# Kernel optimization log

Hardware: AMD Instinct MI355X
Metric: run time of the kernel (lower is better)

Reference implementation:

```python
import jax, jax.numpy as jnp
import numpy as np

B, T, D, H, E = 16, 4096, 256, 512, 8


def setup_inputs() -> dict:
    key = jax.random.key(0)
    ks = jax.random.split(key, 5)
    x = jax.random.normal(ks[0], (B, T, D), dtype=jnp.float32)
    gate_w = jax.random.normal(ks[1], (D, E), dtype=jnp.float32) * 0.02
    gate_b = jnp.zeros((E,), dtype=jnp.float32)
    W1 = jax.random.normal(ks[2], (E, D, H), dtype=jnp.float32) * 0.02
    b1 = jnp.zeros((E, H), dtype=jnp.float32)
    W2 = jax.random.normal(ks[3], (E, H, D), dtype=jnp.float32) * 0.02
    b2 = jnp.zeros((E, D), dtype=jnp.float32)
    return {"x": x, "gate_w": gate_w, "gate_b": gate_b,
            "W1": W1, "b1": b1, "W2": W2, "b2": b2}


def reference(x, gate_w, gate_b, W1, b1, W2, b2):
    Bb, Tt, Dd = x.shape
    Ee = gate_w.shape[1]
    xf = x.reshape(-1, Dd)                       # [N, D]
    N = xf.shape[0]
    logits = xf @ gate_w + gate_b                # [N, E]
    probs = jax.nn.softmax(logits, axis=-1)
    top2_vals, top2_idx = jax.lax.top_k(probs, 2)  # [N, 2]
    # combine weights: w[n, e] = sum_k top2_vals[n,k] * (top2_idx[n,k]==e)
    cw = jnp.zeros((N, Ee), dtype=xf.dtype).at[
        jnp.arange(N)[:, None], top2_idx].add(top2_vals)  # [N, E]

    def step(acc, params):
        w1, bb1, w2, bb2, we = params            # per-expert slices
        h = jax.nn.gelu(xf @ w1 + bb1, approximate=False)  # [N, H]
        y = h @ w2 + bb2                          # [N, D]
        return acc + we[:, None] * y, None

    out, _ = jax.lax.scan(step, jnp.zeros_like(xf),
                          (W1, b1, W2, b2, cw.T))
    return out.reshape(Bb, Tt, Dd)
```

## Files before the change

### kernel.cpp

```cpp
#include <hip/hip_runtime.h>
#include <hip/hip_bf16.h>
#include <math.h>


#define N_TOK 65536
#define D_DIM 256
#define H_DIM 512
#define E_NUM 8
#define TILE_R 32
#define GRID_TILES 4104

typedef __bf16 bf16x8 __attribute__((ext_vector_type(8)));
typedef float f32x4 __attribute__((ext_vector_type(4)));

static __device__ __forceinline__ ushort f2bf(float f) {
    __hip_bfloat16 h = __float2bfloat16(f);
    ushort u;
    __builtin_memcpy(&u, &h, 2);
    return u;
}

static __device__ __forceinline__ float gelu(float v) {
    const float a = fabsf(v) * 0.70710678118654752f;
    const float t = __builtin_amdgcn_rcpf(fmaf(a, 0.47047f, 1.0f));
    const float p = t * fmaf(t, fmaf(t, 0.7478556f, -0.0958798f), 0.3480242f);
    const float er = fmaf(-p, __expf(-a * a), 1.0f);
    const float s = copysignf(er, v);
    return 0.5f * v * (1.0f + s);
}

__global__ __launch_bounds__(256) void pack_w(const float* __restrict__ W1,
                                              const float* __restrict__ W2,
                                              ushort* __restrict__ W1p,
                                              ushort* __restrict__ W2p) {
    const int t = blockIdx.x * 256 + threadIdx.x;
    const int l = t & 63;
    const int lo = l & 15, hi = l >> 4;
    ushort v[8];
    if (blockIdx.y == 0) {
        const int kb = (t >> 6) & 7;
        const int nb = (t >> 9) & 31;
        const int e  = t >> 14;
        const int k0 = kb * 32 + hi * 8;
        const int n  = nb * 16 + lo;
        const float* src = W1 + (size_t)e * D_DIM * H_DIM + n;
        #pragma unroll
        for (int j = 0; j < 8; ++j)
            v[j] = f2bf(src[(size_t)(k0 + j) * H_DIM]);
        *(uint4*)(W1p + (size_t)t * 8) = *(const uint4*)v;
    } else {
        const int kb = (t >> 6) & 15;
        const int nb = (t >> 10) & 15;
        const int e  = t >> 14;
        const int k0 = kb * 32 + hi * 8;
        const int n  = nb * 16 + lo;
        const float* src = W2 + (size_t)e * H_DIM * D_DIM + n;
        #pragma unroll
        for (int j = 0; j < 8; ++j)
            v[j] = f2bf(src[(size_t)(k0 + j) * D_DIM]);
        *(uint4*)(W2p + (size_t)t * 8) = *(const uint4*)v;
    }
}

__global__ __launch_bounds__(256) void gating(const float* __restrict__ x,
                                              const float* __restrict__ gate_w,
                                              const float* __restrict__ gate_b,
                                              ushort* __restrict__ xb,
                                              int* __restrict__ counts,
                                              int* __restrict__ idx_list,
                                              float* __restrict__ wt_list) {
    __shared__ float gws[2048];
    __shared__ int lc[8];
    __shared__ int lbase[8];

    const int tid = threadIdx.x;
    const size_t t0 = (size_t)blockIdx.x * 64;

    for (int i = tid; i < 2048; i += 256) gws[i] = gate_w[i];
    if (tid < 8) lc[tid] = 0;
    __syncthreads();

    const int m = tid >> 2, q = tid & 3;
    const float4* xr = (const float4*)(x + (t0 + m) * D_DIM + q * 64);
    ushort4* xw = (ushort4*)(xb + (t0 + m) * D_DIM + q * 64);

    double lg[8] = {0, 0, 0, 0, 0, 0, 0, 0};
    #pragma unroll
    for (int it = 0; it < 16; ++it) {
        const float4 v = xr[it];
        ushort4 bv;
        bv.x = f2bf(v.x); bv.y = f2bf(v.y); bv.z = f2bf(v.z); bv.w = f2bf(v.w);
        xw[it] = bv;
        const float* g = &gws[(q * 64 + it * 4) * 8];
        const float vv[4] = {v.x, v.y, v.z, v.w};
        #pragma unroll
        for (int j = 0; j < 4; ++j) {
            const double xv = (double)vv[j];
            #pragma unroll
            for (int e2 = 0; e2 < 8; ++e2) lg[e2] += xv * (double)g[j * 8 + e2];
        }
    }
    #pragma unroll
    for (int e2 = 0; e2 < 8; ++e2) {
        lg[e2] += __shfl_xor(lg[e2], 1, 64);
        lg[e2] += __shfl_xor(lg[e2], 2, 64);
    }

    int e0 = 0, e1 = 0, lp0 = 0, lp1 = 0;
    float p0 = 0.f, p1 = 0.f;
    if (q == 0) {
        #pragma unroll
        for (int e2 = 0; e2 < 8; ++e2) lg[e2] += (double)gate_b[e2];
        double b0 = -1e300, b1v = -1e300;
        #pragma unroll
        for (int e2 = 0; e2 < 8; ++e2)
            if (lg[e2] > b0) { b0 = lg[e2]; e0 = e2; }
        e1 = -1;
        #pragma unroll
        for (int e2 = 0; e2 < 8; ++e2)
            if (e2 != e0 && lg[e2] > b1v) { b1v = lg[e2]; e1 = e2; }
        double s = 0;
        #pragma unroll
        for (int e2 = 0; e2 < 8; ++e2) s += exp(lg[e2] - b0);
        p0 = (float)(1.0 / s);
        p1 = (float)(exp(b1v - b0) / s);
        lp0 = atomicAdd(&lc[e0], 1);
        lp1 = atomicAdd(&lc[e1], 1);
    }
    __syncthreads();
    if (tid < 8) lbase[tid] = atomicAdd(&counts[tid], lc[tid]);
    __syncthreads();
    if (q == 0) {
        const int tok = (int)t0 + m;
        const int o0 = e0 * N_TOK + lbase[e0] + lp0;
        idx_list[o0] = tok; wt_list[o0] = p0;
        const int o1 = e1 * N_TOK + lbase[e1] + lp1;
        idx_list[o1] = tok; wt_list[o1] = p1;
    }
}

__global__ __launch_bounds__(512, 4) void moe_expert(const ushort* __restrict__ xb,
                                                     const ushort* __restrict__ W1p,
                                                     const ushort* __restrict__ W2p,
                                                     const float* __restrict__ b1,
                                                     const float* __restrict__ b2,
                                                     const int* __restrict__ counts,
                                                     const int* __restrict__ idx_list,
                                                     const float* __restrict__ wt_list,
                                                     float* __restrict__ out) {
    __shared__ __align__(16) char U[TILE_R * 1024];
    __shared__ int toks[TILE_R];
    __shared__ float wts[TILE_R];

    const int bid = blockIdx.x;
    const int wg = (bid & 7) * (GRID_TILES / 8) + (bid >> 3);

    int e = -1, row0 = 0, cnt = 0, s = 0;
    #pragma unroll
    for (int i = 0; i < 8; ++i) {
        const int c = counts[i];
        const int nt = (c + TILE_R - 1) >> 5;
        if (e < 0 && wg < s + nt) { e = i; row0 = (wg - s) << 5; cnt = c; }
        s += nt;
    }
    if (e < 0) return;
    const int nval = min(TILE_R, cnt - row0);
    const int tid = threadIdx.x;

    char* Xs = U;
    char* Hs = U;

    const int w = tid >> 6;
    const int l = tid & 63;
    const int lo = l & 15, hi = l >> 4;

    if (tid < TILE_R) {
        const bool vld = tid < nval;
        toks[tid] = vld ? idx_list[e * N_TOK + row0 + tid] : 0;
        wts[tid]  = vld ? wt_list[e * N_TOK + row0 + tid] : 0.0f;
    }

    const char* w1b = (const char*)W1p + (size_t)(e * 32 + w * 4) * 8192 + (size_t)l * 16;
    bf16x8 wf[2][4];
    #pragma unroll
    for (int nb = 0; nb < 4; ++nb)
        wf[0][nb] = *(const bf16x8*)(w1b + nb * 8192);

    __syncthreads();

    {
        const int r = tid >> 4, sb = (tid & 15) * 32;
        const char* src = (const char*)(xb + (size_t)toks[r] * D_DIM);
        char* dst = Xs + r * 512;
        const int sw = (r & 7) << 4;
        *(uint4*)(dst + (sb ^ sw)) = *(const uint4*)(src + sb);
        *(uint4*)(dst + ((sb + 16) ^ sw)) = *(const uint4*)(src + sb + 16);
    }
    __syncthreads();

    f32x4 acc1[4][2];
    #pragma unroll
    for (int nb = 0; nb < 4; ++nb)
        #pragma unroll
        for (int tb = 0; tb < 2; ++tb)
            acc1[nb][tb] = (f32x4){0.f, 0.f, 0.f, 0.f};

    #pragma unroll
    for (int ks = 0; ks < 8; ++ks) {
        const int cur = ks & 1, nxt = cur ^ 1;
        if (ks < 7) {
            #pragma unroll
            for (int nb = 0; nb < 4; ++nb)
                wf[nxt][nb] = *(const bf16x8*)(w1b + nb * 8192 + (ks + 1) * 1024);
        }
        #pragma unroll
        for (int tb = 0; tb < 2; ++tb) {
            const int slot = tb * 16 + lo;
            const bf16x8 xf = *(const bf16x8*)(Xs + slot * 512 +
                              ((ks * 64 + hi * 16) ^ ((slot & 7) << 4)));
            __builtin_amdgcn_s_setprio(1);
            #pragma unroll
            for (int nb = 0; nb < 4; ++nb)
                acc1[nb][tb] = __builtin_amdgcn_mfma_f32_16x16x32_bf16(wf[cur][nb], xf, acc1[nb][tb], 0, 0, 0);
            __builtin_amdgcn_s_setprio(0);
        }
    }

    const char* w2b = (const char*)W2p + (size_t)(e * 16 + w * 2) * 16384 + (size_t)l * 16;
    bf16x8 wf2[2][2];
    wf2[0][0] = *(const bf16x8*)(w2b);
    wf2[0][1] = *(const bf16x8*)(w2b + 16384);

    __syncthreads();

    #pragma unroll
    for (int nb = 0; nb < 4; ++nb) {
        const int hc0 = w * 64 + nb * 16 + hi * 4;
        const float4 b1q = *(const float4*)(b1 + e * H_DIM + hc0);
        #pragma unroll
        for (int tb = 0; tb < 2; ++tb) {
            const int slot = tb * 16 + lo;
            ushort4 hv;
            hv.x = f2bf(gelu(acc1[nb][tb][0] + b1q.x));
            hv.y = f2bf(gelu(acc1[nb][tb][1] + b1q.y));
            hv.z = f2bf(gelu(acc1[nb][tb][2] + b1q.z));
            hv.w = f2bf(gelu(acc1[nb][tb][3] + b1q.w));
            *(ushort4*)(Hs + slot * 1024 + ((hc0 * 2) ^ ((slot & 7) << 4))) = hv;
        }
    }
    __syncthreads();

    f32x4 acc2[2][2];
    #pragma unroll
    for (int mi = 0; mi < 2; ++mi)
        #pragma unroll
        for (int ni = 0; ni < 2; ++ni)
            acc2[mi][ni] = (f32x4){0.f, 0.f, 0.f, 0.f};

    #pragma unroll
    for (int ks = 0; ks < 16; ++ks) {
        const int cur = ks & 1, nxt = cur ^ 1;
        if (ks < 15) {
            wf2[nxt][0] = *(const bf16x8*)(w2b + (ks + 1) * 1024);
            wf2[nxt][1] = *(const bf16x8*)(w2b + 16384 + (ks + 1) * 1024);
        }
        #pragma unroll
        for (int mi = 0; mi < 2; ++mi) {
            const int slot = mi * 16 + lo;
            const bf16x8 hf = *(const bf16x8*)(Hs + slot * 1024 +
                              ((ks * 64 + hi * 16) ^ ((slot & 7) << 4)));
            __builtin_amdgcn_s_setprio(1);
            #pragma unroll
            for (int ni = 0; ni < 2; ++ni)
                acc2[mi][ni] = __builtin_amdgcn_mfma_f32_16x16x32_bf16(hf, wf2[cur][ni], acc2[mi][ni], 0, 0, 0);
            __builtin_amdgcn_s_setprio(0);
        }
    }

    #pragma unroll
    for (int ni = 0; ni < 2; ++ni) {
        const int col = w * 32 + ni * 16 + lo;
        const float b2v = b2[e * D_DIM + col];
        #pragma unroll
        for (int mi = 0; mi < 2; ++mi) {
            #pragma unroll
            for (int rg = 0; rg < 4; ++rg) {
                const int r = mi * 16 + hi * 4 + rg;
                if (r < nval) {
                    const float v = (acc2[mi][ni][rg] + b2v) * wts[r];
                    atomicAdd(&out[(size_t)toks[r] * D_DIM + col], v);
                }
            }
        }
    }
}

extern "C" void kernel_launch(void* const* d_in, const int* in_sizes, int n_in,
                              void* d_out, int out_size, void* d_ws, size_t ws_size,
                              hipStream_t stream) {
    const float* x      = (const float*)d_in[0];
    const float* gate_w = (const float*)d_in[1];
    const float* gate_b = (const float*)d_in[2];
    const float* W1     = (const float*)d_in[3];
    const float* b1     = (const float*)d_in[4];
    const float* W2     = (const float*)d_in[5];
    const float* b2     = (const float*)d_in[6];
    float* out = (float*)d_out;

    char* ws = (char*)d_ws;
    ushort* xb      = (ushort*)(ws);
    ushort* W1p     = (ushort*)(ws + 33554432);
    ushort* W2p     = (ushort*)(ws + 35651584);
    int*    idx_lst = (int*)   (ws + 37748736);
    float*  wt_lst  = (float*) (ws + 39845888);
    int*    counts  = (int*)   (ws + 41943040);

    hipMemsetAsync(counts, 0, 32, stream);
    hipMemsetAsync(d_out, 0, (size_t)out_size * sizeof(float), stream);

    pack_w<<<dim3(512, 2), 256, 0, stream>>>(W1, W2, W1p, W2p);
    gating<<<dim3(1024), 256, 0, stream>>>(x, gate_w, gate_b, xb, counts, idx_lst, wt_lst);
    moe_expert<<<dim3(GRID_TILES), 512, 0, stream>>>(xb, W1p, W2p, b1, b2, counts,
                                                     idx_lst, wt_lst, out);
}
```

Measured before the change: 221.1 us.

## Use persistent expert blocks with double-buffered token gather and merge prep kernels

The expert kernel becomes persistent: 512 blocks each walk a contiguous range of tiles, prefetching the next tile's gathered token rows into a second shared buffer while the current tile computes. The W2 prefetch is deepened to a three-slot register ring. Weight packing, gating and output zeroing are merged into a single prep kernel, which removes the output memset and two extra kernel launches. In exchange, occupancy drops from 4 to 2 blocks per SIMD budget and shared memory use goes up, so fewer independent tiles are in flight to hide latency.

```diff
diff --git a/kernel.cpp b/kernel.cpp
--- a/kernel.cpp
+++ b/kernel.cpp
@@ -8,7 +8,7 @@
 #define H_DIM 512
 #define E_NUM 8
 #define TILE_R 32
-#define GRID_TILES 4104
+#define NBLK 512
 
 typedef __bf16 bf16x8 __attribute__((ext_vector_type(8)));
 typedef float f32x4 __attribute__((ext_vector_type(4)));
@@ -29,53 +29,66 @@
     return 0.5f * v * (1.0f + s);
 }
 
-__global__ __launch_bounds__(256) void pack_w(const float* __restrict__ W1,
-                                              const float* __restrict__ W2,
-                                              ushort* __restrict__ W1p,
-                                              ushort* __restrict__ W2p) {
-    const int t = blockIdx.x * 256 + threadIdx.x;
-    const int l = t & 63;
-    const int lo = l & 15, hi = l >> 4;
-    ushort v[8];
-    if (blockIdx.y == 0) {
-        const int kb = (t >> 6) & 7;
-        const int nb = (t >> 9) & 31;
-        const int e  = t >> 14;
-        const int k0 = kb * 32 + hi * 8;
-        const int n  = nb * 16 + lo;
-        const float* src = W1 + (size_t)e * D_DIM * H_DIM + n;
-        #pragma unroll
-        for (int j = 0; j < 8; ++j)
-            v[j] = f2bf(src[(size_t)(k0 + j) * H_DIM]);
-        *(uint4*)(W1p + (size_t)t * 8) = *(const uint4*)v;
-    } else {
-        const int kb = (t >> 6) & 15;
-        const int nb = (t >> 10) & 15;
-        const int e  = t >> 14;
-        const int k0 = kb * 32 + hi * 8;
-        const int n  = nb * 16 + lo;
-        const float* src = W2 + (size_t)e * H_DIM * D_DIM + n;
-        #pragma unroll
-        for (int j = 0; j < 8; ++j)
-            v[j] = f2bf(src[(size_t)(k0 + j) * D_DIM]);
-        *(uint4*)(W2p + (size_t)t * 8) = *(const uint4*)v;
-    }
-}
-
-__global__ __launch_bounds__(256) void gating(const float* __restrict__ x,
-                                              const float* __restrict__ gate_w,
-                                              const float* __restrict__ gate_b,
-                                              ushort* __restrict__ xb,
-                                              int* __restrict__ counts,
-                                              int* __restrict__ idx_list,
-                                              float* __restrict__ wt_list) {
+__global__ __launch_bounds__(256) void prep(const float* __restrict__ x,
+                                            const float* __restrict__ gate_w,
+                                            const float* __restrict__ gate_b,
+                                            const float* __restrict__ W1,
+                                            const float* __restrict__ W2,
+                                            ushort* __restrict__ xb,
+                                            ushort* __restrict__ W1p,
+                                            ushort* __restrict__ W2p,
+                                            int* __restrict__ counts,
+                                            int* __restrict__ idx_list,
+                                            float* __restrict__ wt_list,
+                                            float* __restrict__ out) {
     __shared__ float gws[2048];
     __shared__ int lc[8];
     __shared__ int lbase[8];
 
+    const int bid = blockIdx.x;
     const int tid = threadIdx.x;
-    const size_t t0 = (size_t)blockIdx.x * 64;
-
+
+    if (bid >= 2048) {
+        float4* o4 = (float4*)out;
+        const size_t idx = (size_t)(bid - 2048) * 256 + tid;
+        #pragma unroll
+        for (int k = 0; k < 32; ++k)
+            o4[idx + (size_t)k * 131072] = (float4){0.f, 0.f, 0.f, 0.f};
+        return;
+    }
+    if (bid >= 1024) {
+        const int pid = bid - 1024;
+        const int t = (pid & 511) * 256 + tid;
+        const int l = t & 63;
+        const int lo = l & 15, hi = l >> 4;
+        ushort v[8];
+        if (pid < 512) {
+            const int kb = (t >> 6) & 7;
+            const int nb = (t >> 9) & 31;
+            const int e  = t >> 14;
+            const int k0 = kb * 32 + hi * 8;
+            const int n  = nb * 16 + lo;
+            const float* src = W1 + (size_t)e * D_DIM * H_DIM + n;
+            #pragma unroll
+            for (int j = 0; j < 8; ++j)
+                v[j] = f2bf(src[(size_t)(k0 + j) * H_DIM]);
+            *(uint4*)(W1p + (size_t)t * 8) = *(const uint4*)v;
+        } else {
+            const int kb = (t >> 6) & 15;
+            const int nb = (t >> 10) & 15;
+            const int e  = t >> 14;
+            const int k0 = kb * 32 + hi * 8;
+            const int n  = nb * 16 + lo;
+            const float* src = W2 + (size_t)e * H_DIM * D_DIM + n;
+            #pragma unroll
+            for (int j = 0; j < 8; ++j)
+                v[j] = f2bf(src[(size_t)(k0 + j) * D_DIM]);
+            *(uint4*)(W2p + (size_t)t * 8) = *(const uint4*)v;
+        }
+        return;
+    }
+
+    const size_t t0 = (size_t)bid * 64;
     for (int i = tid; i < 2048; i += 256) gws[i] = gate_w[i];
     if (tid < 8) lc[tid] = 0;
     __syncthreads();
@@ -139,7 +152,7 @@
     }
 }
 
-__global__ __launch_bounds__(512, 4) void moe_expert(const ushort* __restrict__ xb,
+__global__ __launch_bounds__(512, 2) void moe_expert(const ushort* __restrict__ xb,
                                                      const ushort* __restrict__ W1p,
                                                      const ushort* __restrict__ W2p,
                                                      const float* __restrict__ b1,
@@ -148,150 +161,195 @@
                                                      const int* __restrict__ idx_list,
                                                      const float* __restrict__ wt_list,
                                                      float* __restrict__ out) {
-    __shared__ __align__(16) char U[TILE_R * 1024];
-    __shared__ int toks[TILE_R];
-    __shared__ float wts[TILE_R];
-
-    const int bid = blockIdx.x;
-    const int wg = (bid & 7) * (GRID_TILES / 8) + (bid >> 3);
-
-    int e = -1, row0 = 0, cnt = 0, s = 0;
+    __shared__ __align__(16) char Xs[2][TILE_R * 512];
+    __shared__ __align__(16) char Hs[TILE_R * 1024];
+    __shared__ int   toksb[2][TILE_R];
+    __shared__ float wtsb[2][TILE_R];
+
+    const int tid = threadIdx.x;
+    const int w = tid >> 6, l = tid & 63;
+    const int lo = l & 15, hi = l >> 4;
+
+    int cnts[8];
     #pragma unroll
-    for (int i = 0; i < 8; ++i) {
-        const int c = counts[i];
-        const int nt = (c + TILE_R - 1) >> 5;
-        if (e < 0 && wg < s + nt) { e = i; row0 = (wg - s) << 5; cnt = c; }
-        s += nt;
-    }
-    if (e < 0) return;
-    const int nval = min(TILE_R, cnt - row0);
-    const int tid = threadIdx.x;
-
-    char* Xs = U;
-    char* Hs = U;
-
-    const int w = tid >> 6;
-    const int l = tid & 63;
-    const int lo = l & 15, hi = l >> 4;
+    for (int i = 0; i < 8; ++i) cnts[i] = counts[i];
+    int n = 0;
+    #pragma unroll
+    for (int i = 0; i < 8; ++i) n += (cnts[i] + TILE_R - 1) >> 5;
+
+    const int sb = ((blockIdx.x & 7) << 6) + (blockIdx.x >> 3);
+    const int qq = n >> 9, rr2 = n & (NBLK - 1);
+    const int t_begin = sb * qq + min(sb, rr2);
+    const int t_count = qq + (sb < rr2 ? 1 : 0);
+    if (t_count == 0) return;
+
+    auto resolve = [&](int wg, int& e_, int& r0_, int& nv_) {
+        e_ = -1;
+        int s = 0;
+        #pragma unroll
+        for (int i = 0; i < 8; ++i) {
+            const int nt = (cnts[i] + TILE_R - 1) >> 5;
+            if (e_ < 0 && wg < s + nt) {
+                e_ = i; r0_ = (wg - s) << 5; nv_ = min(TILE_R, cnts[i] - r0_);
+            }
+            s += nt;
+        }
+    };
+
+    int e, row0, nval;
+    resolve(t_begin, e, row0, nval);
 
     if (tid < TILE_R) {
-        const bool vld = tid < nval;
-        toks[tid] = vld ? idx_list[e * N_TOK + row0 + tid] : 0;
-        wts[tid]  = vld ? wt_list[e * N_TOK + row0 + tid] : 0.0f;
-    }
-
-    const char* w1b = (const char*)W1p + (size_t)(e * 32 + w * 4) * 8192 + (size_t)l * 16;
-    bf16x8 wf[2][4];
-    #pragma unroll
-    for (int nb = 0; nb < 4; ++nb)
-        wf[0][nb] = *(const bf16x8*)(w1b + nb * 8192);
-
+        const bool v = tid < nval;
+        toksb[0][tid] = v ? idx_list[e * N_TOK + row0 + tid] : 0;
+        wtsb[0][tid]  = v ? wt_list[e * N_TOK + row0 + tid] : 0.f;
+    }
+    {
+        const int r = tid >> 4;
+        const int tk = idx_list[e * N_TOK + row0 + min(r, nval - 1)];
+        const char* src = (const char*)(xb + (size_t)tk * D_DIM) + (tid & 15) * 32;
+        const int bo = (tid & 15) * 32, sw = (r & 7) << 4;
+        const uint4 a0 = *(const uint4*)src;
+        const uint4 a1 = *(const uint4*)(src + 16);
+        *(uint4*)(Xs[0] + r * 512 + (bo ^ sw)) = a0;
+        *(uint4*)(Xs[0] + r * 512 + ((bo + 16) ^ sw)) = a1;
+    }
     __syncthreads();
 
-    {
-        const int r = tid >> 4, sb = (tid & 15) * 32;
-        const char* src = (const char*)(xb + (size_t)toks[r] * D_DIM);
-        char* dst = Xs + r * 512;
-        const int sw = (r & 7) << 4;
-        *(uint4*)(dst + (sb ^ sw)) = *(const uint4*)(src + sb);
-        *(uint4*)(dst + ((sb + 16) ^ sw)) = *(const uint4*)(src + sb + 16);
-    }
-    __syncthreads();
-
-    f32x4 acc1[4][2];
-    #pragma unroll
-    for (int nb = 0; nb < 4; ++nb)
-        #pragma unroll
-        for (int tb = 0; tb < 2; ++tb)
-            acc1[nb][tb] = (f32x4){0.f, 0.f, 0.f, 0.f};
-
-    #pragma unroll
-    for (int ks = 0; ks < 8; ++ks) {
-        const int cur = ks & 1, nxt = cur ^ 1;
-        if (ks < 7) {
-            #pragma unroll
-            for (int nb = 0; nb < 4; ++nb)
-                wf[nxt][nb] = *(const bf16x8*)(w1b + nb * 8192 + (ks + 1) * 1024);
-        }
-        #pragma unroll
-        for (int tb = 0; tb < 2; ++tb) {
-            const int slot = tb * 16 + lo;
-            const bf16x8 xf = *(const bf16x8*)(Xs + slot * 512 +
-                              ((ks * 64 + hi * 16) ^ ((slot & 7) << 4)));
-            __builtin_amdgcn_s_setprio(1);
-            #pragma unroll
-            for (int nb = 0; nb < 4; ++nb)
-                acc1[nb][tb] = __builtin_amdgcn_mfma_f32_16x16x32_bf16(wf[cur][nb], xf, acc1[nb][tb], 0, 0, 0);
-            __builtin_amdgcn_s_setprio(0);
-        }
-    }
-
-    const char* w2b = (const char*)W2p + (size_t)(e * 16 + w * 2) * 16384 + (size_t)l * 16;
-    bf16x8 wf2[2][2];
-    wf2[0][0] = *(const bf16x8*)(w2b);
-    wf2[0][1] = *(const bf16x8*)(w2b + 16384);
-
-    __syncthreads();
-
-    #pragma unroll
-    for (int nb = 0; nb < 4; ++nb) {
-        const int hc0 = w * 64 + nb * 16 + hi * 4;
-        const float4 b1q = *(const float4*)(b1 + e * H_DIM + hc0);
-        #pragma unroll
-        for (int tb = 0; tb < 2; ++tb) {
-            const int slot = tb * 16 + lo;
-            ushort4 hv;
-            hv.x = f2bf(gelu(acc1[nb][tb][0] + b1q.x));
-            hv.y = f2bf(gelu(acc1[nb][tb][1] + b1q.y));
-            hv.z = f2bf(gelu(acc1[nb][tb][2] + b1q.z));
-            hv.w = f2bf(gelu(acc1[nb][tb][3] + b1q.w));
-            *(ushort4*)(Hs + slot * 1024 + ((hc0 * 2) ^ ((slot & 7) << 4))) = hv;
-        }
-    }
-    __syncthreads();
-
-    f32x4 acc2[2][2];
-    #pragma unroll
-    for (int mi = 0; mi < 2; ++mi)
-        #pragma unroll
-        for (int ni = 0; ni < 2; ++ni)
-            acc2[mi][ni] = (f32x4){0.f, 0.f, 0.f, 0.f};
-
-    #pragma unroll
-    for (int ks = 0; ks < 16; ++ks) {
-        const int cur = ks & 1, nxt = cur ^ 1;
-        if (ks < 15) {
-            wf2[nxt][0] = *(const bf16x8*)(w2b + (ks + 1) * 1024);
-            wf2[nxt][1] = *(const bf16x8*)(w2b + 16384 + (ks + 1) * 1024);
-        }
-        #pragma unroll
-        for (int mi = 0; mi < 2; ++mi) {
-            const int slot = mi * 16 + lo;
-            const bf16x8 hf = *(const bf16x8*)(Hs + slot * 1024 +
-                              ((ks * 64 + hi * 16) ^ ((slot & 7) << 4)));
-            __builtin_amdgcn_s_setprio(1);
+    for (int ti = 0; ti < t_count; ++ti) {
+        const int cur = ti & 1;
+        const char* w1b = (const char*)W1p + (size_t)(e * 32 + w * 4) * 8192 + (size_t)l * 16;
+        const char* w2b = (const char*)W2p + (size_t)(e * 16 + w * 2) * 16384 + (size_t)l * 16;
+
+        f32x4 acc1[4][2];
+        #pragma unroll
+        for (int nb = 0; nb < 4; ++nb)
+            #pragma unroll
+            for (int tb = 0; tb < 2; ++tb)
+                acc1[nb][tb] = (f32x4){0.f, 0.f, 0.f, 0.f};
+
+        bf16x8 wf[2][4];
+        #pragma unroll
+        for (int nb = 0; nb < 4; ++nb)
+            wf[0][nb] = *(const bf16x8*)(w1b + nb * 8192);
+
+        #pragma unroll
+        for (int ks = 0; ks < 8; ++ks) {
+            const int cb = ks & 1, nx = cb ^ 1;
+            if (ks < 7) {
+                #pragma unroll
+                for (int nb = 0; nb < 4; ++nb)
+                    wf[nx][nb] = *(const bf16x8*)(w1b + nb * 8192 + (ks + 1) * 1024);
+            }
+            #pragma unroll
+            for (int tb = 0; tb < 2; ++tb) {
+                const int slot = tb * 16 + lo;
+                const bf16x8 xf = *(const bf16x8*)(Xs[cur] + slot * 512 +
+                                  ((ks * 64 + hi * 16) ^ ((slot & 7) << 4)));
+                __builtin_amdgcn_s_setprio(1);
+                #pragma unroll
+                for (int nb = 0; nb < 4; ++nb)
+                    acc1[nb][tb] = __builtin_amdgcn_mfma_f32_16x16x32_bf16(wf[cb][nb], xf, acc1[nb][tb], 0, 0, 0);
+                __builtin_amdgcn_s_setprio(0);
+            }
+        }
+
+        const bool hasN = (ti + 1 < t_count);
+        int e2 = e, row02 = row0, nv2 = nval;
+        uint4 g0 = {0, 0, 0, 0}, g1 = {0, 0, 0, 0};
+        int ntk = 0; float nwt = 0.f;
+        if (hasN) {
+            resolve(t_begin + ti + 1, e2, row02, nv2);
+            const int r = tid >> 4;
+            const int tk2 = idx_list[e2 * N_TOK + row02 + min(r, nv2 - 1)];
+            const char* src = (const char*)(xb + (size_t)tk2 * D_DIM) + (tid & 15) * 32;
+            g0 = *(const uint4*)src;
+            g1 = *(const uint4*)(src + 16);
+            if (tid < TILE_R) {
+                const bool v = tid < nv2;
+                ntk = v ? idx_list[e2 * N_TOK + row02 + tid] : 0;
+                nwt = v ? wt_list[e2 * N_TOK + row02 + tid] : 0.f;
+            }
+        }
+
+        bf16x8 wf2[3][2];
+        wf2[0][0] = *(const bf16x8*)(w2b);
+        wf2[0][1] = *(const bf16x8*)(w2b + 16384);
+        wf2[1][0] = *(const bf16x8*)(w2b + 1024);
+        wf2[1][1] = *(const bf16x8*)(w2b + 16384 + 1024);
+
+        __syncthreads();
+
+        #pragma unroll
+        for (int nb = 0; nb < 4; ++nb) {
+            const int hc0 = w * 64 + nb * 16 + hi * 4;
+            const float4 b1q = *(const float4*)(b1 + e * H_DIM + hc0);
+            #pragma unroll
+            for (int tb = 0; tb < 2; ++tb) {
+                const int slot = tb * 16 + lo;
+                ushort4 hv;
+                hv.x = f2bf(gelu(acc1[nb][tb][0] + b1q.x));
+                hv.y = f2bf(gelu(acc1[nb][tb][1] + b1q.y));
+                hv.z = f2bf(gelu(acc1[nb][tb][2] + b1q.z));
+                hv.w = f2bf(gelu(acc1[nb][tb][3] + b1q.w));
+                *(ushort4*)(Hs + slot * 1024 + ((hc0 * 2) ^ ((slot & 7) << 4))) = hv;
+            }
+        }
+        if (hasN) {
+            const int r = tid >> 4;
+            const int bo = (tid & 15) * 32, sw = (r & 7) << 4;
+            *(uint4*)(Xs[cur ^ 1] + r * 512 + (bo ^ sw)) = g0;
+            *(uint4*)(Xs[cur ^ 1] + r * 512 + ((bo + 16) ^ sw)) = g1;
+            if (tid < TILE_R) { toksb[cur ^ 1][tid] = ntk; wtsb[cur ^ 1][tid] = nwt; }
+        }
+        __syncthreads();
+
+        f32x4 acc2[2][2];
+        #pragma unroll
+        for (int mi = 0; mi < 2; ++mi)
             #pragma unroll
             for (int ni = 0; ni < 2; ++ni)
-                acc2[mi][ni] = __builtin_amdgcn_mfma_f32_16x16x32_bf16(hf, wf2[cur][ni], acc2[mi][ni], 0, 0, 0);
-            __builtin_amdgcn_s_setprio(0);
-        }
-    }
-
-    #pragma unroll
-    for (int ni = 0; ni < 2; ++ni) {
-        const int col = w * 32 + ni * 16 + lo;
-        const float b2v = b2[e * D_DIM + col];
-        #pragma unroll
-        for (int mi = 0; mi < 2; ++mi) {
-            #pragma unroll
-            for (int rg = 0; rg < 4; ++rg) {
-                const int r = mi * 16 + hi * 4 + rg;
-                if (r < nval) {
-                    const float v = (acc2[mi][ni][rg] + b2v) * wts[r];
-                    atomicAdd(&out[(size_t)toks[r] * D_DIM + col], v);
+                acc2[mi][ni] = (f32x4){0.f, 0.f, 0.f, 0.f};
+
+        #pragma unroll
+        for (int ks = 0; ks < 16; ++ks) {
+            const int cb = ks % 3;
+            if (ks < 14) {
+                const int lb = (ks + 2) % 3;
+                wf2[lb][0] = *(const bf16x8*)(w2b + (ks + 2) * 1024);
+                wf2[lb][1] = *(const bf16x8*)(w2b + 16384 + (ks + 2) * 1024);
+            }
+            #pragma unroll
+            for (int mi = 0; mi < 2; ++mi) {
+                const int slot = mi * 16 + lo;
+                const bf16x8 hf = *(const bf16x8*)(Hs + slot * 1024 +
+                                  ((ks * 64 + hi * 16) ^ ((slot & 7) << 4)));
+                __builtin_amdgcn_s_setprio(1);
+                #pragma unroll
+                for (int ni = 0; ni < 2; ++ni)
+                    acc2[mi][ni] = __builtin_amdgcn_mfma_f32_16x16x32_bf16(hf, wf2[cb][ni], acc2[mi][ni], 0, 0, 0);
+                __builtin_amdgcn_s_setprio(0);
+            }
+        }
+
+        #pragma unroll
+        for (int ni = 0; ni < 2; ++ni) {
+            const int col = w * 32 + ni * 16 + lo;
+            const float b2v = b2[e * D_DIM + col];
+            #pragma unroll
+            for (int mi = 0; mi < 2; ++mi) {
+                #pragma unroll
+                for (int rg = 0; rg < 4; ++rg) {
+                    const int r = mi * 16 + hi * 4 + rg;
+                    if (r < nval) {
+                        const float v = (acc2[mi][ni][rg] + b2v) * wtsb[cur][r];
+                        atomicAdd(&out[(size_t)toksb[cur][r] * D_DIM + col], v);
+                    }
                 }
             }
         }
+
+        e = e2; row0 = row02; nval = nv2;
     }
 }
 
@@ -316,10 +374,8 @@
     int*    counts  = (int*)   (ws + 41943040);
 
     hipMemsetAsync(counts, 0, 32, stream);
-    hipMemsetAsync(d_out, 0, (size_t)out_size * sizeof(float), stream);
-
-    pack_w<<<dim3(512, 2), 256, 0, stream>>>(W1, W2, W1p, W2p);
-    gating<<<dim3(1024), 256, 0, stream>>>(x, gate_w, gate_b, xb, counts, idx_lst, wt_lst);
-    moe_expert<<<dim3(GRID_TILES), 512, 0, stream>>>(xb, W1p, W2p, b1, b2, counts,
-                                                     idx_lst, wt_lst, out);
-}
+    prep<<<dim3(2560), 256, 0, stream>>>(x, gate_w, gate_b, W1, W2,
+                                         xb, W1p, W2p, counts, idx_lst, wt_lst, out);
+    moe_expert<<<dim3(NBLK), 512, 0, stream>>>(xb, W1p, W2p, b1, b2, counts,
+                                               idx_lst, wt_lst, out);
+}
```

Measured after the change: 273.4 us. 1.24x slower.

## Group tokens by expert pair and fuse both experts per tile, dropping atomics

Applied to the files above, without the earlier changes.

Tokens are bucketed by their ordered top-2 expert pair so each tile computes both experts' FFNs for the same tokens. The gate weight is folded into the GELU activations and the second GEMM runs over the concatenated hidden of both experts, accumulating the full output in registers. Results are stored directly instead of atomically added, so the output memset goes away. Weight packing is fused into the gating launch and a separate scatter kernel builds the pair-sorted token lists. This costs more shared memory per block (lower occupancy bound) and an extra small kernel.

```diff
diff --git a/kernel.cpp b/kernel.cpp
--- a/kernel.cpp
+++ b/kernel.cpp
@@ -6,9 +6,8 @@
 #define N_TOK 65536
 #define D_DIM 256
 #define H_DIM 512
-#define E_NUM 8
 #define TILE_R 32
-#define GRID_TILES 4104
+#define GRID_TILES 2112
 
 typedef __bf16 bf16x8 __attribute__((ext_vector_type(8)));
 typedef float f32x4 __attribute__((ext_vector_type(4)));
@@ -29,55 +28,58 @@
     return 0.5f * v * (1.0f + s);
 }
 
-__global__ __launch_bounds__(256) void pack_w(const float* __restrict__ W1,
-                                              const float* __restrict__ W2,
-                                              ushort* __restrict__ W1p,
-                                              ushort* __restrict__ W2p) {
-    const int t = blockIdx.x * 256 + threadIdx.x;
-    const int l = t & 63;
-    const int lo = l & 15, hi = l >> 4;
-    ushort v[8];
-    if (blockIdx.y == 0) {
-        const int kb = (t >> 6) & 7;
-        const int nb = (t >> 9) & 31;
-        const int e  = t >> 14;
-        const int k0 = kb * 32 + hi * 8;
-        const int n  = nb * 16 + lo;
-        const float* src = W1 + (size_t)e * D_DIM * H_DIM + n;
-        #pragma unroll
-        for (int j = 0; j < 8; ++j)
-            v[j] = f2bf(src[(size_t)(k0 + j) * H_DIM]);
-        *(uint4*)(W1p + (size_t)t * 8) = *(const uint4*)v;
-    } else {
-        const int kb = (t >> 6) & 15;
-        const int nb = (t >> 10) & 15;
-        const int e  = t >> 14;
-        const int k0 = kb * 32 + hi * 8;
-        const int n  = nb * 16 + lo;
-        const float* src = W2 + (size_t)e * H_DIM * D_DIM + n;
-        #pragma unroll
-        for (int j = 0; j < 8; ++j)
-            v[j] = f2bf(src[(size_t)(k0 + j) * D_DIM]);
-        *(uint4*)(W2p + (size_t)t * 8) = *(const uint4*)v;
-    }
-}
-
-__global__ __launch_bounds__(256) void gating(const float* __restrict__ x,
-                                              const float* __restrict__ gate_w,
-                                              const float* __restrict__ gate_b,
-                                              ushort* __restrict__ xb,
-                                              int* __restrict__ counts,
-                                              int* __restrict__ idx_list,
-                                              float* __restrict__ wt_list) {
+__global__ __launch_bounds__(256) void prep(const float* __restrict__ x,
+                                            const float* __restrict__ gate_w,
+                                            const float* __restrict__ gate_b,
+                                            const float* __restrict__ W1,
+                                            const float* __restrict__ W2,
+                                            ushort* __restrict__ xb,
+                                            ushort* __restrict__ W1p,
+                                            ushort* __restrict__ W2p,
+                                            int* __restrict__ counts,
+                                            int* __restrict__ pid_arr,
+                                            float2* __restrict__ pw_arr) {
     __shared__ float gws[2048];
-    __shared__ int lc[8];
-    __shared__ int lbase[8];
-
+    __shared__ int lc[64];
+
+    const int bid = blockIdx.x;
     const int tid = threadIdx.x;
-    const size_t t0 = (size_t)blockIdx.x * 64;
-
+
+    if (bid >= 1024) {
+        const int pid = bid - 1024;
+        const int t = (pid & 511) * 256 + tid;
+        const int l = t & 63;
+        const int lo = l & 15, hi = l >> 4;
+        ushort v[8];
+        if (pid < 512) {
+            const int kb = (t >> 6) & 7;
+            const int nb = (t >> 9) & 31;
+            const int e  = t >> 14;
+            const int k0 = kb * 32 + hi * 8;
+            const int n  = nb * 16 + lo;
+            const float* src = W1 + (size_t)e * D_DIM * H_DIM + n;
+            #pragma unroll
+            for (int j = 0; j < 8; ++j)
+                v[j] = f2bf(src[(size_t)(k0 + j) * H_DIM]);
+            *(uint4*)(W1p + (size_t)t * 8) = *(const uint4*)v;
+        } else {
+            const int kb = (t >> 6) & 15;
+            const int nb = (t >> 10) & 15;
+            const int e  = t >> 14;
+            const int k0 = kb * 32 + hi * 8;
+            const int n  = nb * 16 + lo;
+            const float* src = W2 + (size_t)e * H_DIM * D_DIM + n;
+            #pragma unroll
+            for (int j = 0; j < 8; ++j)
+                v[j] = f2bf(src[(size_t)(k0 + j) * D_DIM]);
+            *(uint4*)(W2p + (size_t)t * 8) = *(const uint4*)v;
+        }
+        return;
+    }
+
+    const size_t t0 = (size_t)bid * 64;
     for (int i = tid; i < 2048; i += 256) gws[i] = gate_w[i];
-    if (tid < 8) lc[tid] = 0;
+    if (tid < 64) lc[tid] = 0;
     __syncthreads();
 
     const int m = tid >> 2, q = tid & 3;
@@ -106,173 +108,210 @@
         lg[e2] += __shfl_xor(lg[e2], 2, 64);
     }
 
-    int e0 = 0, e1 = 0, lp0 = 0, lp1 = 0;
-    float p0 = 0.f, p1 = 0.f;
     if (q == 0) {
+        int e0 = 0, e1 = -1;
         #pragma unroll
         for (int e2 = 0; e2 < 8; ++e2) lg[e2] += (double)gate_b[e2];
         double b0 = -1e300, b1v = -1e300;
         #pragma unroll
         for (int e2 = 0; e2 < 8; ++e2)
             if (lg[e2] > b0) { b0 = lg[e2]; e0 = e2; }
-        e1 = -1;
         #pragma unroll
         for (int e2 = 0; e2 < 8; ++e2)
             if (e2 != e0 && lg[e2] > b1v) { b1v = lg[e2]; e1 = e2; }
         double s = 0;
         #pragma unroll
         for (int e2 = 0; e2 < 8; ++e2) s += exp(lg[e2] - b0);
-        p0 = (float)(1.0 / s);
-        p1 = (float)(exp(b1v - b0) / s);
-        lp0 = atomicAdd(&lc[e0], 1);
-        lp1 = atomicAdd(&lc[e1], 1);
-    }
-    __syncthreads();
-    if (tid < 8) lbase[tid] = atomicAdd(&counts[tid], lc[tid]);
-    __syncthreads();
-    if (q == 0) {
+        const float p0 = (float)(1.0 / s);
+        const float p1 = (float)(exp(b1v - b0) / s);
+        const int pid = e0 * 8 + e1;
+        atomicAdd(&lc[pid], 1);
         const int tok = (int)t0 + m;
-        const int o0 = e0 * N_TOK + lbase[e0] + lp0;
-        idx_list[o0] = tok; wt_list[o0] = p0;
-        const int o1 = e1 * N_TOK + lbase[e1] + lp1;
-        idx_list[o1] = tok; wt_list[o1] = p1;
-    }
-}
-
-__global__ __launch_bounds__(512, 4) void moe_expert(const ushort* __restrict__ xb,
+        pid_arr[tok] = pid;
+        pw_arr[tok] = make_float2(p0, p1);
+    }
+    __syncthreads();
+    if (tid < 64 && lc[tid]) atomicAdd(&counts[tid], lc[tid]);
+}
+
+__global__ __launch_bounds__(256) void scatter(const int* __restrict__ counts,
+                                               const int* __restrict__ pid_arr,
+                                               const float2* __restrict__ pw_arr,
+                                               int* __restrict__ cursor,
+                                               int* __restrict__ tok_list,
+                                               float* __restrict__ w0l,
+                                               float* __restrict__ w1l) {
+    __shared__ int lcnt[64];
+    __shared__ int lbase[64];
+    const int tid = threadIdx.x;
+    const int t = blockIdx.x * 256 + tid;
+    if (tid < 64) lcnt[tid] = 0;
+    __syncthreads();
+    const int pid = pid_arr[t];
+    const float2 pw = pw_arr[t];
+    const int lpos = atomicAdd(&lcnt[pid], 1);
+    __syncthreads();
+    if (tid < 64) {
+        int s = 0;
+        for (int i = 0; i < tid; ++i) s += counts[i];
+        const int mine = lcnt[tid];
+        lbase[tid] = s + (mine ? atomicAdd(&cursor[tid], mine) : 0);
+    }
+    __syncthreads();
+    const int pos = lbase[pid] + lpos;
+    tok_list[pos] = t;
+    w0l[pos] = pw.x;
+    w1l[pos] = pw.y;
+}
+
+__global__ __launch_bounds__(512, 3) void moe_expert(const ushort* __restrict__ xb,
                                                      const ushort* __restrict__ W1p,
                                                      const ushort* __restrict__ W2p,
                                                      const float* __restrict__ b1,
                                                      const float* __restrict__ b2,
                                                      const int* __restrict__ counts,
-                                                     const int* __restrict__ idx_list,
-                                                     const float* __restrict__ wt_list,
+                                                     const int* __restrict__ tok_list,
+                                                     const float* __restrict__ w0l,
+                                                     const float* __restrict__ w1l,
                                                      float* __restrict__ out) {
-    __shared__ __align__(16) char U[TILE_R * 1024];
-    __shared__ int toks[TILE_R];
-    __shared__ float wts[TILE_R];
-
-    const int bid = blockIdx.x;
-    const int wg = (bid & 7) * (GRID_TILES / 8) + (bid >> 3);
-
-    int e = -1, row0 = 0, cnt = 0, s = 0;
-    #pragma unroll
-    for (int i = 0; i < 8; ++i) {
+    __shared__ __align__(16) char Xs[TILE_R * 512];
+    __shared__ __align__(16) char Hs[TILE_R * 2048];
+
+    int n = 0;
+    for (int i = 0; i < 64; ++i) n += (counts[i] + 31) >> 5;
+    const int qn = n >> 3, rn = n & 7;
+    const int xc = blockIdx.x & 7, ix = blockIdx.x >> 3;
+    if (ix >= qn + (xc < rn ? 1 : 0)) return;
+    const int wg = xc * qn + min(xc, rn) + ix;
+
+    int pid = -1, row0 = 0, nv = 0, gbase = 0;
+    int st = 0, sc = 0;
+    for (int i = 0; i < 64; ++i) {
         const int c = counts[i];
-        const int nt = (c + TILE_R - 1) >> 5;
-        if (e < 0 && wg < s + nt) { e = i; row0 = (wg - s) << 5; cnt = c; }
-        s += nt;
-    }
-    if (e < 0) return;
-    const int nval = min(TILE_R, cnt - row0);
+        const int nt = (c + 31) >> 5;
+        if (pid < 0 && wg < st + nt) { pid = i; row0 = (wg - st) << 5; nv = min(TILE_R, c - row0); gbase = sc; }
+        st += nt; sc += c;
+    }
+    const int ea = pid >> 3, eb = pid & 7;
+    const int gidx = gbase + row0;
+
     const int tid = threadIdx.x;
-
-    char* Xs = U;
-    char* Hs = U;
-
-    const int w = tid >> 6;
-    const int l = tid & 63;
+    const int w = tid >> 6, l = tid & 63;
     const int lo = l & 15, hi = l >> 4;
-
-    if (tid < TILE_R) {
-        const bool vld = tid < nval;
-        toks[tid] = vld ? idx_list[e * N_TOK + row0 + tid] : 0;
-        wts[tid]  = vld ? wt_list[e * N_TOK + row0 + tid] : 0.0f;
-    }
-
-    const char* w1b = (const char*)W1p + (size_t)(e * 32 + w * 4) * 8192 + (size_t)l * 16;
-    bf16x8 wf[2][4];
-    #pragma unroll
-    for (int nb = 0; nb < 4; ++nb)
-        wf[0][nb] = *(const bf16x8*)(w1b + nb * 8192);
-
-    __syncthreads();
+    const int qe = w >> 2, pp = w & 3;
+    const int ew = qe ? eb : ea;
+
+    const float* wl = qe ? w1l : w0l;
+    const float wtv0 = wl[gidx + min(lo, nv - 1)];
+    const float wtv1 = wl[gidx + min(16 + lo, nv - 1)];
 
     {
-        const int r = tid >> 4, sb = (tid & 15) * 32;
-        const char* src = (const char*)(xb + (size_t)toks[r] * D_DIM);
-        char* dst = Xs + r * 512;
-        const int sw = (r & 7) << 4;
-        *(uint4*)(dst + (sb ^ sw)) = *(const uint4*)(src + sb);
-        *(uint4*)(dst + ((sb + 16) ^ sw)) = *(const uint4*)(src + sb + 16);
-    }
-    __syncthreads();
-
-    f32x4 acc1[4][2];
-    #pragma unroll
-    for (int nb = 0; nb < 4; ++nb)
-        #pragma unroll
-        for (int tb = 0; tb < 2; ++tb)
-            acc1[nb][tb] = (f32x4){0.f, 0.f, 0.f, 0.f};
-
-    #pragma unroll
-    for (int ks = 0; ks < 8; ++ks) {
-        const int cur = ks & 1, nxt = cur ^ 1;
-        if (ks < 7) {
-            #pragma unroll
-            for (int nb = 0; nb < 4; ++nb)
-                wf[nxt][nb] = *(const bf16x8*)(w1b + nb * 8192 + (ks + 1) * 1024);
-        }
-        #pragma unroll
-        for (int tb = 0; tb < 2; ++tb) {
-            const int slot = tb * 16 + lo;
-            const bf16x8 xf = *(const bf16x8*)(Xs + slot * 512 +
+        const int r = tid >> 4;
+        const int tk = tok_list[gidx + min(r, nv - 1)];
+        const char* src = (const char*)(xb + (size_t)tk * D_DIM) + (tid & 15) * 32;
+        const int bo = (tid & 15) * 32, sw = (r & 7) << 4;
+        const uint4 a0 = *(const uint4*)src;
+        const uint4 a1 = *(const uint4*)(src + 16);
+        *(uint4*)(Xs + r * 512 + (bo ^ sw)) = a0;
+        *(uint4*)(Xs + r * 512 + ((bo + 16) ^ sw)) = a1;
+    }
+    __syncthreads();
+
+    #pragma unroll
+    for (int hh = 0; hh < 2; ++hh) {
+        const int nbg0 = pp * 8 + hh * 4;
+        const char* w1b = (const char*)W1p + (size_t)(ew * 32 + nbg0) * 8192 + (size_t)l * 16;
+
+        f32x4 acc1[4][2];
+        #pragma unroll
+        for (int nb = 0; nb < 4; ++nb)
+            #pragma unroll
+            for (int tb = 0; tb < 2; ++tb)
+                acc1[nb][tb] = (f32x4){0.f, 0.f, 0.f, 0.f};
+
+        bf16x8 wf[2][4];
+        #pragma unroll
+        for (int nb = 0; nb < 4; ++nb)
+            wf[0][nb] = *(const bf16x8*)(w1b + nb * 8192);
+
+        #pragma unroll
+        for (int ks = 0; ks < 8; ++ks) {
+            const int cb = ks & 1, nx = cb ^ 1;
+            if (ks < 7) {
+                #pragma unroll
+                for (int nb = 0; nb < 4; ++nb)
+                    wf[nx][nb] = *(const bf16x8*)(w1b + nb * 8192 + (ks + 1) * 1024);
+            }
+            #pragma unroll
+            for (int tb = 0; tb < 2; ++tb) {
+                const int slot = tb * 16 + lo;
+                const bf16x8 xf = *(const bf16x8*)(Xs + slot * 512 +
+                                  ((ks * 64 + hi * 16) ^ ((slot & 7) << 4)));
+                __builtin_amdgcn_s_setprio(1);
+                #pragma unroll
+                for (int nb = 0; nb < 4; ++nb)
+                    acc1[nb][tb] = __builtin_amdgcn_mfma_f32_16x16x32_bf16(wf[cb][nb], xf, acc1[nb][tb], 0, 0, 0);
+                __builtin_amdgcn_s_setprio(0);
+            }
+        }
+
+        #pragma unroll
+        for (int nb = 0; nb < 4; ++nb) {
+            const int hc = nbg0 * 16 + nb * 16 + hi * 4;
+            const float4 b1q = *(const float4*)(b1 + ew * H_DIM + hc);
+            const int hgc = qe * H_DIM + hc;
+            #pragma unroll
+            for (int tb = 0; tb < 2; ++tb) {
+                const int slot = tb * 16 + lo;
+                const float wt = tb ? wtv1 : wtv0;
+                ushort4 hv;
+                hv.x = f2bf(gelu(acc1[nb][tb][0] + b1q.x) * wt);
+                hv.y = f2bf(gelu(acc1[nb][tb][1] + b1q.y) * wt);
+                hv.z = f2bf(gelu(acc1[nb][tb][2] + b1q.z) * wt);
+                hv.w = f2bf(gelu(acc1[nb][tb][3] + b1q.w) * wt);
+                *(ushort4*)(Hs + slot * 2048 + ((hgc * 2) ^ ((slot & 7) << 4))) = hv;
+            }
+        }
+    }
+    __syncthreads();
+
+    const char* w2A = (const char*)W2p + (size_t)(ea * 16 + w * 2) * 16384 + (size_t)l * 16;
+    const char* w2B = (const char*)W2p + (size_t)(eb * 16 + w * 2) * 16384 + (size_t)l * 16;
+
+    f32x4 acc2[2][2];
+    #pragma unroll
+    for (int mi = 0; mi < 2; ++mi)
+        #pragma unroll
+        for (int ni = 0; ni < 2; ++ni)
+            acc2[mi][ni] = (f32x4){0.f, 0.f, 0.f, 0.f};
+
+    bf16x8 wf2[3][2];
+    #pragma unroll
+    for (int ni = 0; ni < 2; ++ni) {
+        wf2[0][ni] = *(const bf16x8*)(w2A + ni * 16384);
+        wf2[1][ni] = *(const bf16x8*)(w2A + ni * 16384 + 1024);
+    }
+
+    #pragma unroll
+    for (int ks = 0; ks < 32; ++ks) {
+        const int cb = ks % 3;
+        if (ks < 30) {
+            const int lb = (ks + 2) % 3;
+            const int kk = ks + 2;
+            const char* base = (kk < 16) ? w2A : w2B;
+            const int kloc = kk & 15;
+            wf2[lb][0] = *(const bf16x8*)(base + kloc * 1024);
+            wf2[lb][1] = *(const bf16x8*)(base + 16384 + kloc * 1024);
+        }
+        #pragma unroll
+        for (int mi = 0; mi < 2; ++mi) {
+            const int slot = mi * 16 + lo;
+            const bf16x8 hf = *(const bf16x8*)(Hs + slot * 2048 +
                               ((ks * 64 + hi * 16) ^ ((slot & 7) << 4)));
             __builtin_amdgcn_s_setprio(1);
             #pragma unroll
-            for (int nb = 0; nb < 4; ++nb)
-                acc1[nb][tb] = __builtin_amdgcn_mfma_f32_16x16x32_bf16(wf[cur][nb], xf, acc1[nb][tb], 0, 0, 0);
-            __builtin_amdgcn_s_setprio(0);
-        }
-    }
-
-    const char* w2b = (const char*)W2p + (size_t)(e * 16 + w * 2) * 16384 + (size_t)l * 16;
-    bf16x8 wf2[2][2];
-    wf2[0][0] = *(const bf16x8*)(w2b);
-    wf2[0][1] = *(const bf16x8*)(w2b + 16384);
-
-    __syncthreads();
-
-    #pragma unroll
-    for (int nb = 0; nb < 4; ++nb) {
-        const int hc0 = w * 64 + nb * 16 + hi * 4;
-        const float4 b1q = *(const float4*)(b1 + e * H_DIM + hc0);
-        #pragma unroll
-        for (int tb = 0; tb < 2; ++tb) {
-            const int slot = tb * 16 + lo;
-            ushort4 hv;
-            hv.x = f2bf(gelu(acc1[nb][tb][0] + b1q.x));
-            hv.y = f2bf(gelu(acc1[nb][tb][1] + b1q.y));
-            hv.z = f2bf(gelu(acc1[nb][tb][2] + b1q.z));
-            hv.w = f2bf(gelu(acc1[nb][tb][3] + b1q.w));
-            *(ushort4*)(Hs + slot * 1024 + ((hc0 * 2) ^ ((slot & 7) << 4))) = hv;
-        }
-    }
-    __syncthreads();
-
-    f32x4 acc2[2][2];
-    #pragma unroll
-    for (int mi = 0; mi < 2; ++mi)
-        #pragma unroll
-        for (int ni = 0; ni < 2; ++ni)
-            acc2[mi][ni] = (f32x4){0.f, 0.f, 0.f, 0.f};
-
-    #pragma unroll
-    for (int ks = 0; ks < 16; ++ks) {
-        const int cur = ks & 1, nxt = cur ^ 1;
-        if (ks < 15) {
-            wf2[nxt][0] = *(const bf16x8*)(w2b + (ks + 1) * 1024);
-            wf2[nxt][1] = *(const bf16x8*)(w2b + 16384 + (ks + 1) * 1024);
-        }
-        #pragma unroll
-        for (int mi = 0; mi < 2; ++mi) {
-            const int slot = mi * 16 + lo;
-            const bf16x8 hf = *(const bf16x8*)(Hs + slot * 1024 +
-                              ((ks * 64 + hi * 16) ^ ((slot & 7) << 4)));
-            __builtin_amdgcn_s_setprio(1);
-            #pragma unroll
             for (int ni = 0; ni < 2; ++ni)
-                acc2[mi][ni] = __builtin_amdgcn_mfma_f32_16x16x32_bf16(hf, wf2[cur][ni], acc2[mi][ni], 0, 0, 0);
+                acc2[mi][ni] = __builtin_amdgcn_mfma_f32_16x16x32_bf16(hf, wf2[cb][ni], acc2[mi][ni], 0, 0, 0);
             __builtin_amdgcn_s_setprio(0);
         }
     }
@@ -280,15 +319,17 @@
     #pragma unroll
     for (int ni = 0; ni < 2; ++ni) {
         const int col = w * 32 + ni * 16 + lo;
-        const float b2v = b2[e * D_DIM + col];
+        const float b2a = b2[ea * D_DIM + col];
+        const float b2b = b2[eb * D_DIM + col];
         #pragma unroll
         for (int mi = 0; mi < 2; ++mi) {
             #pragma unroll
             for (int rg = 0; rg < 4; ++rg) {
                 const int r = mi * 16 + hi * 4 + rg;
-                if (r < nval) {
-                    const float v = (acc2[mi][ni][rg] + b2v) * wts[r];
-                    atomicAdd(&out[(size_t)toks[r] * D_DIM + col], v);
+                if (r < nv) {
+                    const int tok = tok_list[gidx + r];
+                    const float v = acc2[mi][ni][rg] + w0l[gidx + r] * b2a + w1l[gidx + r] * b2b;
+                    out[(size_t)tok * D_DIM + col] = v;
                 }
             }
         }
@@ -311,15 +352,20 @@
     ushort* xb      = (ushort*)(ws);
     ushort* W1p     = (ushort*)(ws + 33554432);
     ushort* W2p     = (ushort*)(ws + 35651584);
-    int*    idx_lst = (int*)   (ws + 37748736);
-    float*  wt_lst  = (float*) (ws + 39845888);
-    int*    counts  = (int*)   (ws + 41943040);
-
-    hipMemsetAsync(counts, 0, 32, stream);
-    hipMemsetAsync(d_out, 0, (size_t)out_size * sizeof(float), stream);
-
-    pack_w<<<dim3(512, 2), 256, 0, stream>>>(W1, W2, W1p, W2p);
-    gating<<<dim3(1024), 256, 0, stream>>>(x, gate_w, gate_b, xb, counts, idx_lst, wt_lst);
+    int*    pid_arr = (int*)   (ws + 37748736);
+    float2* pw_arr  = (float2*)(ws + 38010880);
+    int*    tok_lst = (int*)   (ws + 38535168);
+    float*  w0l     = (float*) (ws + 38797312);
+    float*  w1l     = (float*) (ws + 39059456);
+    int*    counts  = (int*)   (ws + 39321600);
+    int*    cursor  = (int*)   (ws + 39321856);
+
+    hipMemsetAsync(counts, 0, 512, stream);
+
+    prep<<<dim3(2048), 256, 0, stream>>>(x, gate_w, gate_b, W1, W2,
+                                         xb, W1p, W2p, counts, pid_arr, pw_arr);
+    scatter<<<dim3(256), 256, 0, stream>>>(counts, pid_arr, pw_arr, cursor,
+                                           tok_lst, w0l, w1l);
     moe_expert<<<dim3(GRID_TILES), 512, 0, stream>>>(xb, W1p, W2p, b1, b2, counts,
-                                                     idx_lst, wt_lst, out);
-}
+                                                     tok_lst, w0l, w1l, out);
+}
```

Measured after the change: 207.7 us. -6.1%, faster.
